# Performance work log

Measured on AMD Instinct MI355X. Metric: run time of the kernel, lower is better.

## Reference

```python
import jax, jax.numpy as jnp
import numpy as np


def _gcn_conv(x, src, dst, norm, W, b, n_nodes):
    # GCNConv: h = x @ W; out[i] = sum_{j->i} norm_ji * h[j] + b
    h = x @ W                                   # [N, out]
    msg = h[src] * norm[:, None]                # [E+N, out]
    return jax.ops.segment_sum(msg, dst, num_segments=n_nodes) + b


def _sym_norm(edge_index, n_nodes, dtype):
    # add self-loops, compute deg^{-1/2}[src] * deg^{-1/2}[dst]
    loops = jnp.arange(n_nodes, dtype=edge_index.dtype)
    src = jnp.concatenate([edge_index[0], loops])
    dst = jnp.concatenate([edge_index[1], loops])
    deg = jax.ops.segment_sum(jnp.ones_like(dst, dtype), dst, num_segments=n_nodes)
    dinv = jnp.where(deg > 0, jax.lax.rsqrt(deg), jnp.zeros((), dtype))
    norm = dinv[src] * dinv[dst]
    return src, dst, norm


def setup_inputs() -> dict:
    key = jax.random.key(0)
    k1, k2, k3, k4 = jax.random.split(key, 4)
    N, E = 50000, 800000
    IN, HID, OUT = 256, 256, 128
    x = jax.random.normal(k1, (N, IN), dtype=jnp.float32)
    edge_index = jax.random.randint(k2, (2, E), 0, N, dtype=jnp.int64)
    W1 = jax.random.normal(k3, (IN, HID), dtype=jnp.float32) * (1.0 / np.sqrt(IN))
    b1 = jnp.zeros((HID,), jnp.float32)
    W2 = jax.random.normal(k4, (HID, OUT), dtype=jnp.float32) * (1.0 / np.sqrt(HID))
    b2 = jnp.zeros((OUT,), jnp.float32)
    return {"x": x, "edge_index": edge_index, "W1": W1, "b1": b1, "W2": W2, "b2": b2}


def reference(x, edge_index, W1, b1, W2, b2):
    n_nodes = x.shape[0]
    src, dst, norm = _sym_norm(edge_index, n_nodes, x.dtype)
    h = jax.nn.relu(_gcn_conv(x, src, dst, norm, W1, b1, n_nodes))
    z = jax.nn.relu(_gcn_conv(h, src, dst, norm, W2, b2, n_nodes))
    return z
```

## Files before the change

### kernel.cpp

```cpp
#include <hip/hip_runtime.h>
#include <hip/hip_bf16.h>
#include <cstdint>
#include <cstddef>


typedef float f32x4 __attribute__((ext_vector_type(4)));
typedef _Float16 f16x8 __attribute__((ext_vector_type(8)));

#define AS1 __attribute__((address_space(1)))
#define AS3 __attribute__((address_space(3)))
#define BCAP 6144

__global__ __launch_bounds__(256) void k_scatter(const int* __restrict__ src,
                                                 const int* __restrict__ dst,
                                                 int* __restrict__ cursor,
                                                 long long* __restrict__ ebuf, int E) {
    __shared__ int hist[256];
    const int t = threadIdx.x;
    const int chunk = (E + gridDim.x - 1) / gridDim.x;
    const int lo = blockIdx.x * chunk;
    const int hi = (lo + chunk < E) ? lo + chunk : E;
    hist[t] = 0;
    __syncthreads();
    for (int e = lo + t; e < hi; e += 256) atomicAdd(&hist[dst[e] >> 8], 1);
    __syncthreads();
    int h = hist[t];
    __syncthreads();
    if (h > 0) hist[t] = atomicAdd(&cursor[t], h);
    __syncthreads();
    for (int e = lo + t; e < hi; e += 256) {
        int d = dst[e];
        int r = atomicAdd(&hist[d >> 8], 1);
        ebuf[(size_t)(d >> 8) * BCAP + r] = ((long long)src[e] << 32) | (unsigned int)d;
    }
}

__global__ __launch_bounds__(256) void k_bktscan(const int* __restrict__ cursor,
                                                 int* __restrict__ bstart) {
    __shared__ int s[256];
    const int t = threadIdx.x;
    int v = cursor[t];
    s[t] = v;
    __syncthreads();
    for (int off = 1; off < 256; off <<= 1) {
        int u = (t >= off) ? s[t - off] : 0;
        __syncthreads();
        s[t] += u;
        __syncthreads();
    }
    bstart[t] = s[t] - v;
}

__global__ __launch_bounds__(256) void k_bktsort(const long long* __restrict__ ebuf,
                                                 const int* __restrict__ cursor,
                                                 const int* __restrict__ bstart,
                                                 int* __restrict__ rowptr,
                                                 int* __restrict__ colv,
                                                 float* __restrict__ dinv,
                                                 int N, int E) {
    __shared__ int hist[256], s[256], cur[256];
    const int b = blockIdx.x, t = threadIdx.x;
    const int cnt = cursor[b], gbase = bstart[b];
    const long long* eb = ebuf + (size_t)b * BCAP;
    hist[t] = 0;
    __syncthreads();
    for (int i = t; i < cnt; i += 256) atomicAdd(&hist[(int)(eb[i] & 255)], 1);
    __syncthreads();
    int h = hist[t];
    s[t] = h;
    __syncthreads();
    for (int off = 1; off < 256; off <<= 1) {
        int u = (t >= off) ? s[t - off] : 0;
        __syncthreads();
        s[t] += u;
        __syncthreads();
    }
    const int base = s[t] - h;
    cur[t] = gbase + base;
    const int d = b * 256 + t;
    if (d < N) {
        rowptr[d] = gbase + base;
        dinv[d] = rsqrtf((float)(h + 1));
    }
    if (b == 0 && t == 0) rowptr[N] = E;
    __syncthreads();
    for (int i = t; i < cnt; i += 256) {
        long long p = eb[i];
        int r = atomicAdd(&cur[(int)(p & 255)], 1);
        colv[r] = (int)(p >> 32);
    }
}

__global__ __launch_bounds__(256) void k_thalf2(const float* __restrict__ W1,
                                                _Float16* __restrict__ T1,
                                                const float* __restrict__ W2,
                                                _Float16* __restrict__ T2,
                                                int R1, int C1, int R2, int C2) {
    const float* src; _Float16* dh; int R, C;
    if (blockIdx.z == 0) { src = W1; dh = T1; R = R1; C = C1; }
    else                 { src = W2; dh = T2; R = R2; C = C2; }
    if ((int)blockIdx.x * 64 >= C || (int)blockIdx.y * 64 >= R) return;
    __shared__ float tile[64][65];
    int r0 = blockIdx.y * 64, c0 = blockIdx.x * 64;
    for (int i = threadIdx.x; i < 4096; i += 256) {
        int r = i >> 6, c = i & 63;
        tile[r][c] = src[(size_t)(r0 + r) * C + c0 + c];
    }
    __syncthreads();
    for (int i = threadIdx.x; i < 4096; i += 256) {
        int r = i >> 6, c = i & 63;
        dh[(size_t)(c0 + r) * R + r0 + c] = (_Float16)tile[c][r];
    }
}

__global__ __launch_bounds__(256) void k_gemm1(const float* __restrict__ X,
                                               const _Float16* __restrict__ B,
                                               const float* __restrict__ scale,
                                               _Float16* __restrict__ C,
                                               int M, int K, int Nc) {
    __shared__ __align__(16) _Float16 lds[2 * 128 * 64];
    _Float16* Afl = lds;
    _Float16* Bfl = lds + 8192;
    const int tid = threadIdx.x;
    const int m0 = blockIdx.x * 128, n0 = blockIdx.y * 128;
    const int w = tid >> 6, lane = tid & 63;
    const int wr = w >> 1, wc = w & 1;
    const int fr = lane & 15, kg = lane >> 4;

    const int arow = tid >> 1;
    const int kf = (tid & 1) * 32;
    int rgA = m0 + arow; if (rgA >= M) rgA = M - 1;
    const float* ap0 = X + (size_t)rgA * K + kf;

    f32x4 acc[4][4] = {};

    for (int k0 = 0; k0 < K; k0 += 64) {
#pragma unroll
        for (int c = 0; c < 4; ++c) {
            const int r = c * 4 + w;
            const int wch = r * 64 + lane;
            const int row = wch >> 3, slot = wch & 7;
            const _Float16* gp = B + (size_t)(n0 + row) * K + k0 + ((slot ^ (row & 7)) << 3);
            __builtin_amdgcn_global_load_lds((const AS1 void*)gp,
                                             (AS3 void*)(Bfl + (size_t)r * 512), 16, 0, 0);
        }
        {
            const float* ap = ap0 + k0;
#pragma unroll
            for (int c2 = 0; c2 < 4; ++c2) {
                float4 q0 = *(const float4*)(ap + c2 * 8);
                float4 q1 = *(const float4*)(ap + c2 * 8 + 4);
                f16x8 hv;
                hv[0] = (_Float16)q0.x; hv[1] = (_Float16)q0.y;
                hv[2] = (_Float16)q0.z; hv[3] = (_Float16)q0.w;
                hv[4] = (_Float16)q1.x; hv[5] = (_Float16)q1.y;
                hv[6] = (_Float16)q1.z; hv[7] = (_Float16)q1.w;
                const int s = (tid & 1) * 4 + c2;
                *(f16x8*)&Afl[arow * 64 + ((s ^ (arow & 7)) << 3)] = hv;
            }
        }
        __syncthreads();
#pragma unroll
        for (int kc = 0; kc < 2; ++kc) {
            f16x8 a_f[4], b_f[4];
#pragma unroll
            for (int i = 0; i < 4; ++i) {
                const int ar = wr * 64 + i * 16 + fr;
                a_f[i] = *(const f16x8*)&Afl[ar * 64 + (((kc * 4 + kg) ^ (ar & 7)) << 3)];
                const int br = wc * 64 + i * 16 + fr;
                b_f[i] = *(const f16x8*)&Bfl[br * 64 + (((kc * 4 + kg) ^ (br & 7)) << 3)];
            }
#pragma unroll
            for (int i = 0; i < 4; ++i)
#pragma unroll
                for (int j = 0; j < 4; ++j)
                    acc[i][j] = __builtin_amdgcn_mfma_f32_16x16x32_f16(a_f[i], b_f[j], acc[i][j], 0, 0, 0);
        }
        __syncthreads();
    }
#pragma unroll
    for (int i = 0; i < 4; ++i) {
        const int rbase = m0 + wr * 64 + i * 16 + (lane >> 4) * 4;
#pragma unroll
        for (int r = 0; r < 4; ++r) {
            const int row = rbase + r;
            if (row < M) {
                const float s = scale[row];
#pragma unroll
                for (int j = 0; j < 4; ++j) {
                    const int col = n0 + wc * 64 + j * 16 + fr;
                    const size_t o = ((size_t)(col >> 6) * M + row) * 64 + (col & 63);
                    C[o] = (_Float16)(acc[i][j][r] * s);
                }
            }
        }
    }
}

__global__ __launch_bounds__(256) void k_gemm2(const _Float16* __restrict__ Ap,
                                               const _Float16* __restrict__ Bp,
                                               const float* __restrict__ scale,
                                               _Float16* __restrict__ C,
                                               int M, int K, int Nc) {
    __shared__ __align__(16) _Float16 lds[2 * 128 * 64];
    const int tid = threadIdx.x;
    const int m0 = blockIdx.x * 128, n0 = blockIdx.y * 128;
    const int w = tid >> 6, lane = tid & 63;
    const int wr = w >> 1, wc = w & 1;
    const int fr = lane & 15, kg = lane >> 4;

    f32x4 acc[4][4] = {};

    for (int k0 = 0; k0 < K; k0 += 64) {
#pragma unroll
        for (int c = 0; c < 8; ++c) {
            const int r = c * 4 + w;
            const int p = r >> 4;
            const int wch = (r & 15) * 64 + lane;
            const int row = wch >> 3, slot = wch & 7;
            const int swz = (slot ^ (row & 7)) << 3;
            const _Float16* gp;
            if (p == 0) {
                int rg = m0 + row; if (rg >= M) rg = M - 1;
                gp = Ap + (size_t)rg * K + k0 + swz;
            } else {
                gp = Bp + (size_t)(n0 + row) * K + k0 + swz;
            }
            __builtin_amdgcn_global_load_lds((const AS1 void*)gp,
                                             (AS3 void*)(lds + (size_t)r * 512), 16, 0, 0);
        }
        __syncthreads();
#pragma unroll
        for (int kc = 0; kc < 2; ++kc) {
            f16x8 a_f[4], b_f[4];
#pragma unroll
            for (int i = 0; i < 4; ++i) {
                const int ar = wr * 64 + i * 16 + fr;
                a_f[i] = *(const f16x8*)&lds[ar * 64 + (((kc * 4 + kg) ^ (ar & 7)) << 3)];
                const int br = wc * 64 + i * 16 + fr;
                b_f[i] = *(const f16x8*)&lds[8192 + br * 64 + (((kc * 4 + kg) ^ (br & 7)) << 3)];
            }
#pragma unroll
            for (int i = 0; i < 4; ++i)
#pragma unroll
                for (int j = 0; j < 4; ++j)
                    acc[i][j] = __builtin_amdgcn_mfma_f32_16x16x32_f16(a_f[i], b_f[j], acc[i][j], 0, 0, 0);
        }
        __syncthreads();
    }
#pragma unroll
    for (int i = 0; i < 4; ++i) {
        const int rbase = m0 + wr * 64 + i * 16 + (lane >> 4) * 4;
#pragma unroll
        for (int r = 0; r < 4; ++r) {
            const int row = rbase + r;
            if (row < M) {
                const float s = scale[row];
#pragma unroll
                for (int j = 0; j < 4; ++j) {
                    const int col = n0 + wc * 64 + j * 16 + fr;
                    const size_t o = ((size_t)(col >> 6) * M + row) * 64 + (col & 63);
                    C[o] = (_Float16)(acc[i][j][r] * s);
                }
            }
        }
    }
}

template <int NSLICE, bool OUTF16>
__global__ __launch_bounds__(256) void k_agg_gr(const _Float16* __restrict__ tbl0,
                                                const int* __restrict__ rowptr,
                                                const int* __restrict__ colv,
                                                const float* __restrict__ dinv,
                                                const float* __restrict__ bias,
                                                float* __restrict__ outf,
                                                _Float16* __restrict__ outh, int n) {
    constexpr int F = NSLICE * 64;
    const int slice = blockIdx.x;
    const int g = threadIdx.x >> 3;
    const int li = threadIdx.x & 7;
    const int fb = li * 8;
    const int wid = blockIdx.y * 32 + g;
    if (wid >= n) return;
    const _Float16* tbl = tbl0 + (size_t)slice * n * 64 + fb;

    float acc[8];
    {
        f16x8 v = *(const f16x8*)(tbl + (size_t)wid * 64);
#pragma unroll
        for (int j = 0; j < 8; ++j) acc[j] = (float)v[j];
    }
    const int p0 = rowptr[wid], p1 = rowptr[wid + 1];
    int p = p0;
    for (; p + 4 <= p1; p += 4) {
        int s0 = colv[p], s1 = colv[p + 1], s2 = colv[p + 2], s3 = colv[p + 3];
        f16x8 v0 = *(const f16x8*)(tbl + (size_t)s0 * 64);
        f16x8 v1 = *(const f16x8*)(tbl + (size_t)s1 * 64);
        f16x8 v2 = *(const f16x8*)(tbl + (size_t)s2 * 64);
        f16x8 v3 = *(const f16x8*)(tbl + (size_t)s3 * 64);
#pragma unroll
        for (int j = 0; j < 8; ++j)
            acc[j] += ((float)v0[j] + (float)v1[j]) + ((float)v2[j] + (float)v3[j]);
    }
    for (; p < p1; ++p) {
        f16x8 v = *(const f16x8*)(tbl + (size_t)colv[p] * 64);
#pragma unroll
        for (int j = 0; j < 8; ++j) acc[j] += (float)v[j];
    }
    const float di = dinv[wid];
    float r[8];
#pragma unroll
    for (int j = 0; j < 8; ++j) {
        float t = di * acc[j] + bias[slice * 64 + fb + j];
        r[j] = t > 0.f ? t : 0.f;
    }
    const size_t o = (size_t)wid * F + slice * 64 + fb;
    if constexpr (OUTF16) {
        f16x8 hv;
#pragma unroll
        for (int j = 0; j < 8; ++j) hv[j] = (_Float16)r[j];
        *(f16x8*)(outh + o) = hv;
    } else {
        float* op = outf + o;
        *(float4*)(op)     = make_float4(r[0], r[1], r[2], r[3]);
        *(float4*)(op + 4) = make_float4(r[4], r[5], r[6], r[7]);
    }
}

extern "C" void kernel_launch(void* const* d_in, const int* in_sizes, int n_in,
                              void* d_out, int out_size, void* d_ws, size_t ws_size,
                              hipStream_t stream) {
    const float* x  = (const float*)d_in[0];
    const int*   ei = (const int*)d_in[1];
    const float* W1 = (const float*)d_in[2];
    const float* b1 = (const float*)d_in[3];
    const float* W2 = (const float*)d_in[4];
    const float* b2 = (const float*)d_in[5];

    const int HID = in_sizes[3];
    const int IN  = in_sizes[2] / HID;
    const int OUT = in_sizes[5];
    const int N   = in_sizes[0] / IN;
    const int E   = in_sizes[1] / 2;

    const int* src = ei;
    const int* dst = ei + E;

    char* wsb = (char*)d_ws;
    size_t off = 0;
    auto carve = [&](size_t bytes) -> char* {
        char* p = wsb + off;
        off += (bytes + 255) & ~(size_t)255;
        return p;
    };
    _Float16* h1  = (_Float16*)carve((size_t)N * HID * 2);
    _Float16* hsb = (_Float16*)carve((size_t)N * HID * 2);
    _Float16* gsb = (_Float16*)carve((size_t)N * OUT * 2);
    float* dinv   = (float*)carve((size_t)N * 4);
    int*   rowptr = (int*)carve((size_t)(N + 1) * 4);
    int*   colv   = (int*)carve((size_t)E * 4);
    long long* ebuf = (long long*)carve((size_t)256 * BCAP * 8);
    int*   cursor = (int*)carve(1024);
    int*   bstart = (int*)carve(1024);
    _Float16* W1Th = (_Float16*)carve((size_t)IN * HID * 2);
    _Float16* W2Th = (_Float16*)carve((size_t)HID * OUT * 2);
    (void)ws_size; (void)n_in; (void)out_size;

    const int nbkt = (N + 255) >> 8;
    const int ybN = (N + 31) / 32;

    hipMemsetAsync(cursor, 0, 1024, stream);
    k_scatter<<<256, 256, 0, stream>>>(src, dst, cursor, ebuf, E);
    k_bktscan<<<1, 256, 0, stream>>>(cursor, bstart);
    k_bktsort<<<nbkt, 256, 0, stream>>>(ebuf, cursor, bstart, rowptr, colv, dinv, N, E);

    k_thalf2<<<dim3(4, 4, 2), 256, 0, stream>>>(W1, W1Th, W2, W2Th, IN, HID, HID, OUT);

    k_gemm1<<<dim3((N + 127) / 128, HID / 128), 256, 0, stream>>>(
        x, W1Th, dinv, hsb, N, IN, HID);
    k_agg_gr<4, true><<<dim3(4, ybN), 256, 0, stream>>>(
        hsb, rowptr, colv, dinv, b1, nullptr, h1, N);
    k_gemm2<<<dim3((N + 127) / 128, OUT / 128), 256, 0, stream>>>(
        h1, W2Th, dinv, gsb, N, HID, OUT);
    k_agg_gr<2, false><<<dim3(2, ybN), 256, 0, stream>>>(
        gsb, rowptr, colv, dinv, b2, (float*)d_out, nullptr, N);
}
```

Before: 162.3 us.

## Sort nodes by degree to balance gather-aggregation work across wavefronts

Measured after the change: 434.1 us. 2.67x slower.

```diff
diff --git a/kernel.cpp b/kernel.cpp
--- a/kernel.cpp
+++ b/kernel.cpp
@@ -57,6 +57,7 @@
                                                  int* __restrict__ rowptr,
                                                  int* __restrict__ colv,
                                                  float* __restrict__ dinv,
+                                                 int* __restrict__ dbin,
                                                  int N, int E) {
     __shared__ int hist[256], s[256], cur[256];
     const int b = blockIdx.x, t = threadIdx.x;
@@ -81,6 +82,7 @@
     if (d < N) {
         rowptr[d] = gbase + base;
         dinv[d] = rsqrtf((float)(h + 1));
+        atomicAdd(&dbin[h > 63 ? 63 : h], 1);
     }
     if (b == 0 && t == 0) rowptr[N] = E;
     __syncthreads();
@@ -88,6 +90,34 @@
         long long p = eb[i];
         int r = atomicAdd(&cur[(int)(p & 255)], 1);
         colv[r] = (int)(p >> 32);
+    }
+}
+
+__global__ __launch_bounds__(64) void k_dscan(const int* __restrict__ dbin,
+                                              int* __restrict__ dcur) {
+    __shared__ int s[64];
+    const int t = threadIdx.x;
+    int v = dbin[t];
+    s[t] = v;
+    __syncthreads();
+    for (int off = 1; off < 64; off <<= 1) {
+        int u = (t >= off) ? s[t - off] : 0;
+        __syncthreads();
+        s[t] += u;
+        __syncthreads();
+    }
+    dcur[t] = s[t] - v;
+}
+
+__global__ __launch_bounds__(256) void k_dperm(const int* __restrict__ rowptr,
+                                               int* __restrict__ dcur,
+                                               int* __restrict__ perm, int N) {
+    int i = blockIdx.x * 256 + threadIdx.x;
+    if (i < N) {
+        int deg = rowptr[i + 1] - rowptr[i];
+        int bin = deg > 63 ? 63 : deg;
+        int pos = atomicAdd(&dcur[bin], 1);
+        perm[pos] = i;
     }
 }
 
@@ -271,6 +301,7 @@
 __global__ __launch_bounds__(256) void k_agg_gr(const _Float16* __restrict__ tbl0,
                                                 const int* __restrict__ rowptr,
                                                 const int* __restrict__ colv,
+                                                const int* __restrict__ perm,
                                                 const float* __restrict__ dinv,
                                                 const float* __restrict__ bias,
                                                 float* __restrict__ outf,
@@ -280,8 +311,9 @@
     const int g = threadIdx.x >> 3;
     const int li = threadIdx.x & 7;
     const int fb = li * 8;
-    const int wid = blockIdx.y * 32 + g;
-    if (wid >= n) return;
+    const int idx = blockIdx.y * 32 + g;
+    if (idx >= n) return;
+    const int wid = perm[idx];
     const _Float16* tbl = tbl0 + (size_t)slice * n * 64 + fb;
 
     float acc[8];
@@ -361,27 +393,33 @@
     int*   colv   = (int*)carve((size_t)E * 4);
     long long* ebuf = (long long*)carve((size_t)256 * BCAP * 8);
     int*   cursor = (int*)carve(1024);
+    int*   dbin   = (int*)carve(256);
+    int*   dcur   = (int*)carve(256);
     int*   bstart = (int*)carve(1024);
+    int*   perm   = (int*)carve((size_t)N * 4);
     _Float16* W1Th = (_Float16*)carve((size_t)IN * HID * 2);
     _Float16* W2Th = (_Float16*)carve((size_t)HID * OUT * 2);
     (void)ws_size; (void)n_in; (void)out_size;
 
     const int nbkt = (N + 255) >> 8;
-    const int ybN = (N + 31) / 32;
-
-    hipMemsetAsync(cursor, 0, 1024, stream);
+    const int nbN  = (N + 255) / 256;
+    const int ybN  = (N + 31) / 32;
+
+    hipMemsetAsync(cursor, 0, 1536, stream);
     k_scatter<<<256, 256, 0, stream>>>(src, dst, cursor, ebuf, E);
     k_bktscan<<<1, 256, 0, stream>>>(cursor, bstart);
-    k_bktsort<<<nbkt, 256, 0, stream>>>(ebuf, cursor, bstart, rowptr, colv, dinv, N, E);
+    k_bktsort<<<nbkt, 256, 0, stream>>>(ebuf, cursor, bstart, rowptr, colv, dinv, dbin, N, E);
+    k_dscan<<<1, 64, 0, stream>>>(dbin, dcur);
+    k_dperm<<<nbN, 256, 0, stream>>>(rowptr, dcur, perm, N);
 
     k_thalf2<<<dim3(4, 4, 2), 256, 0, stream>>>(W1, W1Th, W2, W2Th, IN, HID, HID, OUT);
 
     k_gemm1<<<dim3((N + 127) / 128, HID / 128), 256, 0, stream>>>(
         x, W1Th, dinv, hsb, N, IN, HID);
     k_agg_gr<4, true><<<dim3(4, ybN), 256, 0, stream>>>(
-        hsb, rowptr, colv, dinv, b1, nullptr, h1, N);
+        hsb, rowptr, colv, perm, dinv, b1, nullptr, h1, N);
     k_gemm2<<<dim3((N + 127) / 128, OUT / 128), 256, 0, stream>>>(
         h1, W2Th, dinv, gsb, N, HID, OUT);
     k_agg_gr<2, false><<<dim3(2, ybN), 256, 0, stream>>>(
-        gsb, rowptr, colv, dinv, b2, (float*)d_out, nullptr, N);
-}
+        gsb, rowptr, colv, perm, dinv, b2, (float*)d_out, nullptr, N);
+}
```
